# Optimization experiments

Hardware: AMD Instinct MI355X
Metric: run time of the kernel (lower is better)

The kernel has to match this reference:

```python
import jax, jax.numpy as jnp
import numpy as np

B, L, D, H, DH = 2, 2048, 768, 12, 3072
HD = D // H          # head dim = 64
EPS = 1e-6
SCALE = float(np.sqrt(HD))


def setup_inputs() -> dict:
    key = jax.random.key(0)
    ks = jax.random.split(key, 24)
    w = lambda k, shape: jax.random.normal(k, shape, jnp.float32) * 0.02
    # RoPE angles: [L, HD//2]
    inv_freq = 1.0 / (10000.0 ** (jnp.arange(HD // 2, dtype=jnp.float32) / (HD // 2)))
    ang = jnp.arange(L, dtype=jnp.float32)[:, None] * inv_freq[None, :]
    return {
        "x": jax.random.normal(ks[0], (B, L, D), jnp.float32),
        "c": jax.random.normal(ks[1], (B, D), jnp.float32),
        "freqs_cos": jnp.cos(ang),
        "freqs_sin": jnp.sin(ang),
        "W_q": w(ks[2], (D, D)), "W_k": w(ks[3], (D, D)),
        "W_v": w(ks[4], (D, D)), "W_o": w(ks[5], (D, D)),
        "cond_w1": w(ks[6], (D, DH)), "cond_b1": jnp.zeros((DH,), jnp.float32),
        "cond_w2": w(ks[7], (DH, D)), "cond_b2": jnp.zeros((D,), jnp.float32),
        "attn_norm_w": jnp.ones((D,), jnp.float32),
        "attn_alpha": w(ks[8], (D, D)), "attn_beta": w(ks[9], (D, D)),
        "attn_gamma": w(ks[10], (D, D)),
        "ffn_gate": w(ks[11], (D, DH)), "ffn_hidden": w(ks[12], (D, DH)),
        "ffn_out": w(ks[13], (DH, D)),
        "ffn_norm_w": jnp.ones((D,), jnp.float32),
        "ffn_beta": w(ks[14], (D, D)), "ffn_gamma": w(ks[15], (D, D)),
    }


def _rms_norm(x, w):
    return w * x * jax.lax.rsqrt(jnp.mean(x * x, axis=-1, keepdims=True) + EPS)


def _rope(x, cos, sin):
    # x: [b, n, l, hd]; complex pairs are consecutive (even, odd) lanes
    x0, x1 = x[..., 0::2], x[..., 1::2]
    c, s = cos[None, None], sin[None, None]          # [1,1,l,hd//2]
    r0 = x0 * c - x1 * s
    r1 = x0 * s + x1 * c
    return jnp.stack([r0, r1], axis=-1).reshape(x.shape)


def _attention(h, cos, sin, W_q, W_k, W_v, W_o):
    b, l, d = h.shape
    split = lambda y: y.reshape(b, l, H, HD).transpose(0, 2, 1, 3)  # b n l hd
    q = _rope(split(h @ W_q), cos, sin)
    k = _rope(split(h @ W_k), cos, sin)
    v = split(h @ W_v)
    scores = jnp.einsum("bnld,bnmd->bnlm", q, k) / SCALE
    attn = jax.nn.softmax(scores, axis=-1)
    o = jnp.einsum("bnlm,bnmd->bnld", attn, v)
    return o.transpose(0, 2, 1, 3).reshape(b, l, d) @ W_o


def reference(x, c, freqs_cos, freqs_sin, W_q, W_k, W_v, W_o,
              cond_w1, cond_b1, cond_w2, cond_b2,
              attn_norm_w, attn_alpha, attn_beta, attn_gamma,
              ffn_gate, ffn_hidden, ffn_out, ffn_norm_w, ffn_beta, ffn_gamma):
    # conditioning embedding
    c2 = jax.nn.silu(c @ cond_w1 + cond_b1) @ cond_w2 + cond_b2   # [b, d]
    mod = lambda W: (c2 @ W)[:, None]                              # [b, 1, d]
    # attention sub-block with AdaLN modulation + alpha gating
    h = _rms_norm(x, attn_norm_w) * mod(attn_gamma) + mod(attn_beta)
    x = x + _attention(h, freqs_cos, freqs_sin, W_q, W_k, W_v, W_o) * mod(attn_alpha)
    # SwiGLU FFN sub-block (original gates the residual by ffn_gamma, not alpha)
    h = _rms_norm(x, ffn_norm_w) * mod(ffn_gamma) + mod(ffn_beta)
    ff = (jax.nn.silu(h @ ffn_gate) * (h @ ffn_hidden)) @ ffn_out
    return x + ff * mod(ffn_gamma)
```

## Files before the change

kernel.cpp:

```cpp
#include <hip/hip_runtime.h>

typedef unsigned short u16;
typedef __attribute__((ext_vector_type(8))) short short8;
typedef __attribute__((ext_vector_type(4))) float f32x4;

#define L_SEQ 2048
#define NHEAD 12
#define KVB 128

__device__ __forceinline__ u16 f2bf(float f) {
    union { float f; unsigned u; } x; x.f = f;
    unsigned r = x.u + 0x7fffu + ((x.u >> 16) & 1u);
    return (u16)(r >> 16);
}
__device__ __forceinline__ float bf2f(u16 u) {
    union { unsigned u; float f; } x; x.u = ((unsigned)u) << 16;
    return x.f;
}
__device__ __forceinline__ float silu_f(float x) { return x / (1.f + __expf(-x)); }

__device__ __forceinline__ void gload16(const u16* g, u16* l) {
    __builtin_amdgcn_global_load_lds(
        (const __attribute__((address_space(1))) void*)g,
        (__attribute__((address_space(3))) void*)l, 16, 0, 0);
}

__global__ __launch_bounds__(256) void transpose_convert4(
    const float* __restrict__ S0, const float* __restrict__ S1,
    const float* __restrict__ S2, const float* __restrict__ S3,
    u16* __restrict__ D0, u16* __restrict__ D1, u16* __restrict__ D2, u16* __restrict__ D3,
    int K, int N)
{
    const float* W = (blockIdx.z == 0) ? S0 : (blockIdx.z == 1) ? S1 : (blockIdx.z == 2) ? S2 : S3;
    u16* Wt = (blockIdx.z == 0) ? D0 : (blockIdx.z == 1) ? D1 : (blockIdx.z == 2) ? D2 : D3;
    __shared__ float t[32][33];
    int tx = threadIdx.x & 31, ty = threadIdx.x >> 5;
    int n0 = blockIdx.x * 32, k0 = blockIdx.y * 32;
#pragma unroll
    for (int i = 0; i < 4; i++)
        t[ty + 8 * i][tx] = W[(size_t)(k0 + ty + 8 * i) * N + n0 + tx];
    __syncthreads();
#pragma unroll
    for (int i = 0; i < 4; i++)
        Wt[(size_t)(n0 + ty + 8 * i) * K + k0 + tx] = f2bf(t[tx][ty + 8 * i]);
}

__global__ __launch_bounds__(256) void cond_mlp1(
    const float* __restrict__ c, const float* __restrict__ w1, float* __restrict__ part)
{
    int j = blockIdx.x * 256 + threadIdx.x;
    int d0 = blockIdx.y * 96;
    float a0 = 0.f, a1 = 0.f;
    for (int d = d0; d < d0 + 96; ++d) {
        float w = w1[(size_t)d * 3072 + j];
        a0 += c[d] * w;
        a1 += c[768 + d] * w;
    }
    part[(size_t)(blockIdx.y * 2 + 0) * 3072 + j] = a0;
    part[(size_t)(blockIdx.y * 2 + 1) * 3072 + j] = a1;
}

__global__ __launch_bounds__(256) void cond_mlp2(
    const float* __restrict__ part, const float* __restrict__ b1,
    const float* __restrict__ w2, float* __restrict__ c2part)
{
    __shared__ float hid[2][384];
    const int tid = threadIdx.x;
    const int d0 = blockIdx.y * 384;
    for (int i = tid; i < 768; i += 256) {
        int b = i / 384, dd = i - b * 384;
        float s = b1[d0 + dd];
#pragma unroll
        for (int p = 0; p < 8; p++) s += part[(size_t)(p * 2 + b) * 3072 + d0 + dd];
        hid[b][dd] = silu_f(s);
    }
    __syncthreads();
    int jj = tid & 63, kc = tid >> 6;
    int j = blockIdx.x * 64 + jj;
    float a0 = 0.f, a1 = 0.f;
    for (int dd = kc * 96; dd < kc * 96 + 96; ++dd) {
        float w = w2[(size_t)(d0 + dd) * 768 + j];
        a0 += hid[0][dd] * w;
        a1 += hid[1][dd] * w;
    }
    __shared__ float r0[256], r1[256];
    r0[tid] = a0; r1[tid] = a1;
    __syncthreads();
    if (kc == 0) {
        a0 = r0[jj] + r0[64 + jj] + r0[128 + jj] + r0[192 + jj];
        a1 = r1[jj] + r1[64 + jj] + r1[128 + jj] + r1[192 + jj];
        c2part[(size_t)(blockIdx.y * 2 + 0) * 768 + j] = a0;
        c2part[(size_t)(blockIdx.y * 2 + 1) * 768 + j] = a1;
    }
}

__global__ __launch_bounds__(256) void mod_gemm(
    const float* __restrict__ c2part, const float* __restrict__ b2,
    const float* __restrict__ W0, const float* __restrict__ W1,
    const float* __restrict__ W2, const float* __restrict__ W3,
    const float* __restrict__ W4, float* __restrict__ out)
{
    __shared__ float c2s[2][768];
    const int tid = threadIdx.x;
    for (int i = tid; i < 1536; i += 256) {
        int b = i / 768, d = i - b * 768;
        float s = b2[d];
#pragma unroll
        for (int p = 0; p < 8; p++) s += c2part[(size_t)(p * 2 + b) * 768 + d];
        c2s[b][d] = s;
    }
    __syncthreads();
    int w = blockIdx.y;
    const float* W = (w == 0) ? W0 : (w == 1) ? W1 : (w == 2) ? W2 : (w == 3) ? W3 : W4;
    int jj = tid & 63, kc = tid >> 6;
    int j = blockIdx.x * 64 + jj;
    float a0 = 0.f, a1 = 0.f;
    for (int d = kc * 192; d < kc * 192 + 192; ++d) {
        float ww = W[(size_t)d * 768 + j];
        a0 += c2s[0][d] * ww;
        a1 += c2s[1][d] * ww;
    }
    __shared__ float r0[256], r1[256];
    r0[tid] = a0; r1[tid] = a1;
    __syncthreads();
    if (kc == 0) {
        a0 = r0[jj] + r0[64 + jj] + r0[128 + jj] + r0[192 + jj];
        a1 = r1[jj] + r1[64 + jj] + r1[128 + jj] + r1[192 + jj];
        out[(size_t)(w * 2 + 0) * 768 + j] = a0;
        out[(size_t)(w * 2 + 1) * 768 + j] = a1;
    }
}

__global__ __launch_bounds__(256) void rmsnorm_mod(
    const float* __restrict__ xin, const float* __restrict__ nw,
    const float* __restrict__ gamma, const float* __restrict__ beta,
    u16* __restrict__ hout)
{
    int row = blockIdx.x;
    int b = row >> 11;
    const float* xr = xin + (size_t)row * 768;
    int t = threadIdx.x;
    float v0 = xr[t], v1 = xr[t + 256], v2 = xr[t + 512];
    float ss = v0 * v0 + v1 * v1 + v2 * v2;
#pragma unroll
    for (int m = 1; m < 64; m <<= 1) ss += __shfl_xor(ss, m);
    __shared__ float red[4];
    if ((t & 63) == 0) red[t >> 6] = ss;
    __syncthreads();
    float tot = red[0] + red[1] + red[2] + red[3];
    float rr = rsqrtf(tot * (1.f / 768.f) + 1e-6f);
    u16* ho = hout + (size_t)row * 768;
    const float* g = gamma + (size_t)b * 768;
    const float* be = beta + (size_t)b * 768;
#pragma unroll
    for (int i = 0; i < 3; i++) {
        int col = t + i * 256;
        float v = (i == 0) ? v0 : (i == 1) ? v1 : v2;
        ho[col] = f2bf(v * rr * nw[col] * g[col] + be[col]);
    }
}

template<int BM, int WM, int MODE>
__global__ __launch_bounds__(256) void gemm_bf16(
    const u16* __restrict__ A, const u16* __restrict__ Bt,
    float* __restrict__ Cf, u16* __restrict__ Cb,
    const float* __restrict__ X, const float* __restrict__ coef,
    int M, int N, int K)
{
    constexpr int MR = WM / 16, NR = 4;
    __shared__ __align__(16) u16 As[2][BM * 32];
    __shared__ __align__(16) u16 Bs[2][128 * 32];
    const int tid = threadIdx.x;
    const int lane = tid & 63, wid = tid >> 6;
    const int lo = lane & 15, hi = lane >> 4;
    const int bm = blockIdx.x * BM, bn = blockIdx.y * 128;
    const int wrow = (wid >> 1) * WM, wcol = (wid & 1) * 64;

    f32x4 acc[MR][NR];
#pragma unroll
    for (int a = 0; a < MR; a++)
#pragma unroll
        for (int b = 0; b < NR; b++)
            acc[a][b] = (f32x4){0.f, 0.f, 0.f, 0.f};

    auto stage = [&](int buf, int k0) {
#pragma unroll
        for (int p = 0; p < BM / 64; p++) {
            int ch = tid + p * 256;
            gload16(A + (size_t)(bm + (ch >> 2)) * K + k0 + (ch & 3) * 8, &As[buf][ch * 8]);
        }
#pragma unroll
        for (int p = 0; p < 2; p++) {
            int ch = tid + p * 256;
            gload16(Bt + (size_t)(bn + (ch >> 2)) * K + k0 + (ch & 3) * 8, &Bs[buf][ch * 8]);
        }
    };

    stage(0, 0);
    int cur = 0;
    const int NT = K >> 5;
    for (int t = 0; t < NT; t++) {
        __syncthreads();
        if (t + 1 < NT) stage(cur ^ 1, (t + 1) * 32);
        short8 af[MR], bfr[NR];
#pragma unroll
        for (int mi = 0; mi < MR; mi++)
            af[mi] = *(const short8*)(&As[cur][(wrow + mi * 16 + lo) * 32 + hi * 8]);
#pragma unroll
        for (int nj = 0; nj < NR; nj++)
            bfr[nj] = *(const short8*)(&Bs[cur][(wcol + nj * 16 + lo) * 32 + hi * 8]);
        __builtin_amdgcn_s_setprio(1);
#pragma unroll
        for (int mi = 0; mi < MR; mi++)
#pragma unroll
            for (int nj = 0; nj < NR; nj++)
                acc[mi][nj] = __builtin_amdgcn_mfma_f32_16x16x32_bf16(af[mi], bfr[nj], acc[mi][nj], 0, 0, 0);
        __builtin_amdgcn_s_setprio(0);
        cur ^= 1;
    }
#pragma unroll
    for (int mi = 0; mi < MR; mi++)
#pragma unroll
        for (int nj = 0; nj < NR; nj++)
#pragma unroll
            for (int i = 0; i < 4; i++) {
                int row = bm + wrow + mi * 16 + hi * 4 + i;
                int col = bn + wcol + nj * 16 + lo;
                size_t idx = (size_t)row * N + col;
                float v = acc[mi][nj][i];
                if (MODE == 1) {
                    Cb[idx] = f2bf(v);
                } else {
                    int b = row >> 11;
                    Cf[idx] = X[idx] + v * coef[(size_t)b * N + col];
                }
            }
}

__global__ __launch_bounds__(256) void gemm_ffn1(
    const u16* __restrict__ A, const u16* __restrict__ Gt, const u16* __restrict__ Ht,
    u16* __restrict__ ff, int M, int N, int K)
{
    __shared__ __align__(16) u16 As[2][128 * 32];
    __shared__ __align__(16) u16 Gs[2][64 * 32];
    __shared__ __align__(16) u16 Hs[2][64 * 32];
    const int tid = threadIdx.x;
    const int lane = tid & 63, wid = tid >> 6;
    const int lo = lane & 15, hi = lane >> 4;
    const int bm = blockIdx.x * 128, bn = blockIdx.y * 64;
    const int wrow = (wid >> 1) * 64, wcol = (wid & 1) * 32;

    f32x4 ag[4][2], ah[4][2];
#pragma unroll
    for (int a = 0; a < 4; a++)
#pragma unroll
        for (int b = 0; b < 2; b++) {
            ag[a][b] = (f32x4){0.f, 0.f, 0.f, 0.f};
            ah[a][b] = (f32x4){0.f, 0.f, 0.f, 0.f};
        }

    auto stage = [&](int buf, int k0) {
#pragma unroll
        for (int p = 0; p < 2; p++) {
            int ch = tid + p * 256;
            gload16(A + (size_t)(bm + (ch >> 2)) * K + k0 + (ch & 3) * 8, &As[buf][ch * 8]);
        }
        {
            int ch = tid;
            gload16(Gt + (size_t)(bn + (ch >> 2)) * K + k0 + (ch & 3) * 8, &Gs[buf][ch * 8]);
            gload16(Ht + (size_t)(bn + (ch >> 2)) * K + k0 + (ch & 3) * 8, &Hs[buf][ch * 8]);
        }
    };

    stage(0, 0);
    int cur = 0;
    const int NT = K >> 5;
    for (int t = 0; t < NT; t++) {
        __syncthreads();
        if (t + 1 < NT) stage(cur ^ 1, (t + 1) * 32);
        short8 af[4], gf[2], hf[2];
#pragma unroll
        for (int mi = 0; mi < 4; mi++)
            af[mi] = *(const short8*)(&As[cur][(wrow + mi * 16 + lo) * 32 + hi * 8]);
#pragma unroll
        for (int nj = 0; nj < 2; nj++) {
            gf[nj] = *(const short8*)(&Gs[cur][(wcol + nj * 16 + lo) * 32 + hi * 8]);
            hf[nj] = *(const short8*)(&Hs[cur][(wcol + nj * 16 + lo) * 32 + hi * 8]);
        }
        __builtin_amdgcn_s_setprio(1);
#pragma unroll
        for (int mi = 0; mi < 4; mi++)
#pragma unroll
            for (int nj = 0; nj < 2; nj++) {
                ag[mi][nj] = __builtin_amdgcn_mfma_f32_16x16x32_bf16(af[mi], gf[nj], ag[mi][nj], 0, 0, 0);
                ah[mi][nj] = __builtin_amdgcn_mfma_f32_16x16x32_bf16(af[mi], hf[nj], ah[mi][nj], 0, 0, 0);
            }
        __builtin_amdgcn_s_setprio(0);
        cur ^= 1;
    }
#pragma unroll
    for (int mi = 0; mi < 4; mi++)
#pragma unroll
        for (int nj = 0; nj < 2; nj++)
#pragma unroll
            for (int i = 0; i < 4; i++) {
                int row = bm + wrow + mi * 16 + hi * 4 + i;
                int col = bn + wcol + nj * 16 + lo;
                ff[(size_t)row * N + col] = f2bf(silu_f(ag[mi][nj][i]) * ah[mi][nj][i]);
            }
}

__global__ __launch_bounds__(256) void rope_reshape(
    const u16* __restrict__ qr, const u16* __restrict__ kr, const u16* __restrict__ vr,
    const float* __restrict__ fc, const float* __restrict__ fs,
    u16* __restrict__ qo, u16* __restrict__ ko, u16* __restrict__ vt)
{
    const float QSCALE = 0.125f * 1.44269504f;
    __shared__ u16 Vl[64 * 64];
    const int tid = threadIdx.x;
    const int bh = blockIdx.y, lt = blockIdx.x;
    const int b = bh / NHEAD, h = bh % NHEAD;
    const int l0 = lt * 64;
    const int lrow = tid >> 2, ch = tid & 3;

    const size_t srow = ((size_t)(b * L_SEQ + l0 + lrow)) * 2304 + h * 64 + ch * 16;
    const size_t drow = ((size_t)(bh * L_SEQ + l0 + lrow)) * 64 + ch * 16;

    float cs[8], sn[8];
#pragma unroll
    for (int i = 0; i < 8; i++) {
        cs[i] = fc[(l0 + lrow) * 32 + ch * 8 + i];
        sn[i] = fs[(l0 + lrow) * 32 + ch * 8 + i];
    }
    union { int4 v4[2]; u16 s[16]; } iv, ov;
    iv.v4[0] = *(const int4*)(qr + srow); iv.v4[1] = *(const int4*)(qr + srow + 8);
#pragma unroll
    for (int i = 0; i < 8; i++) {
        float x0 = bf2f(iv.s[2 * i]), x1 = bf2f(iv.s[2 * i + 1]);
        ov.s[2 * i]     = f2bf((x0 * cs[i] - x1 * sn[i]) * QSCALE);
        ov.s[2 * i + 1] = f2bf((x0 * sn[i] + x1 * cs[i]) * QSCALE);
    }
    *(int4*)(qo + drow) = ov.v4[0]; *(int4*)(qo + drow + 8) = ov.v4[1];
    iv.v4[0] = *(const int4*)(kr + srow); iv.v4[1] = *(const int4*)(kr + srow + 8);
#pragma unroll
    for (int i = 0; i < 8; i++) {
        float x0 = bf2f(iv.s[2 * i]), x1 = bf2f(iv.s[2 * i + 1]);
        ov.s[2 * i]     = f2bf(x0 * cs[i] - x1 * sn[i]);
        ov.s[2 * i + 1] = f2bf(x0 * sn[i] + x1 * cs[i]);
    }
    *(int4*)(ko + drow) = ov.v4[0]; *(int4*)(ko + drow + 8) = ov.v4[1];
    iv.v4[0] = *(const int4*)(vr + srow); iv.v4[1] = *(const int4*)(vr + srow + 8);
#pragma unroll
    for (int e = 0; e < 16; e++) {
        int d = ch * 16 + e;
        Vl[d * 64 + (lrow ^ (((d >> 3) & 7) << 3))] = iv.s[e];
    }
    __syncthreads();
    const int d = tid >> 2;
    const int key = ((d >> 3) & 7) << 3;
    int4 o0 = *(const int4*)(&Vl[d * 64 + ((ch * 16) ^ key)]);
    int4 o1 = *(const int4*)(&Vl[d * 64 + ((ch * 16 + 8) ^ key)]);
    u16* vd = vt + ((size_t)bh * 64 + d) * L_SEQ + l0 + ch * 16;
    *(int4*)(vd) = o0; *(int4*)(vd + 8) = o1;
}

__global__ __launch_bounds__(256) void attn_fwd(
    const u16* __restrict__ q, const u16* __restrict__ k, const u16* __restrict__ vt,
    u16* __restrict__ outp)
{
    __shared__ __align__(16) u16 Kb[KVB * 64];
    __shared__ __align__(16) u16 Vb[64 * KVB];
    const int tid = threadIdx.x;
    const int lane = tid & 63, wid = tid >> 6;
    const int lo = lane & 15, hi = lane >> 4;
    const int lid = blockIdx.x;
    const int xcd = lid & 7, li = lid >> 3;
    const int bh = xcd * 3 + (li >> 5);
    const int qt = li & 31;
    const int b = bh / NHEAD, h = bh % NHEAD;
    const int q0 = qt * 64 + wid * 16;
    const u16* qb = q + ((size_t)bh * L_SEQ + q0) * 64;
    const u16* kbase = k + (size_t)bh * L_SEQ * 64;
    const u16* vbase = vt + (size_t)bh * 64 * L_SEQ;

    short8 qa0 = *(const short8*)(qb + lo * 64 + hi * 8);
    short8 qa1 = *(const short8*)(qb + lo * 64 + 32 + hi * 8);

    f32x4 oacc[4];
#pragma unroll
    for (int dt = 0; dt < 4; dt++) oacc[dt] = (f32x4){0.f, 0.f, 0.f, 0.f};
    float m_ = -1e30f, ls = 0.f;

    const int rk = tid >> 3, gk = tid & 7;
    const u16* ka = kbase + (size_t)rk * 64 + ((gk ^ (rk & 7)) * 8);
    const int rv = tid >> 4, gv = tid & 15;
    const u16* va = vbase + (size_t)rv * L_SEQ + ((gv ^ (rv & 15)) * 8);
    u16* kdst = &Kb[tid * 8];
    u16* vdst = &Vb[tid * 8];

    int4 kr0, kr1, kr2, kr3, vr0, vr1, vr2, vr3;
    kr0 = *(const int4*)(ka);
    kr1 = *(const int4*)(ka + 2048);
    kr2 = *(const int4*)(ka + 4096);
    kr3 = *(const int4*)(ka + 6144);
    vr0 = *(const int4*)(va);
    vr1 = *(const int4*)(va + 32768);
    vr2 = *(const int4*)(va + 65536);
    vr3 = *(const int4*)(va + 98304);

    const int NT = L_SEQ / KVB;
    u16* pw = &Kb[wid * 2048];
    const int pkey = lo << 3;
    for (int t = 0; t < NT; t++) {
        __syncthreads();
        *(int4*)(kdst)         = kr0;
        *(int4*)(kdst + 2048)  = kr1;
        *(int4*)(kdst + 4096)  = kr2;
        *(int4*)(kdst + 6144)  = kr3;
        *(int4*)(vdst)         = vr0;
        *(int4*)(vdst + 2048)  = vr1;
        *(int4*)(vdst + 4096)  = vr2;
        *(int4*)(vdst + 6144)  = vr3;
        __syncthreads();
        if (t + 1 < NT) {
            int kv0 = (t + 1) * KVB;
            const u16* kan = ka + (size_t)kv0 * 64;
            const u16* van = va + kv0;
            kr0 = *(const int4*)(kan);
            kr1 = *(const int4*)(kan + 2048);
            kr2 = *(const int4*)(kan + 4096);
            kr3 = *(const int4*)(kan + 6144);
            vr0 = *(const int4*)(van);
            vr1 = *(const int4*)(van + 32768);
            vr2 = *(const int4*)(van + 65536);
            vr3 = *(const int4*)(van + 98304);
        }
        f32x4 s[8];
#pragma unroll
        for (int nt = 0; nt < 8; nt++) {
            int kr_ = nt * 16 + lo;
            const u16* kp = &Kb[kr_ * 64];
            int key = (kr_ & 7) << 3;
            short8 kf0 = *(const short8*)(kp + ((hi * 8) ^ key));
            short8 kf1 = *(const short8*)(kp + ((32 + hi * 8) ^ key));
            __builtin_amdgcn_s_setprio(1);
            f32x4 z = (f32x4){0.f, 0.f, 0.f, 0.f};
            z = __builtin_amdgcn_mfma_f32_16x16x32_bf16(kf0, qa0, z, 0, 0, 0);
            s[nt] = __builtin_amdgcn_mfma_f32_16x16x32_bf16(kf1, qa1, s[nt] = z, 0, 0, 0);
            __builtin_amdgcn_s_setprio(0);
        }
        float t0 = fmaxf(fmaxf(s[0][0], s[0][1]), fmaxf(s[0][2], s[0][3]));
        float t1 = fmaxf(fmaxf(s[1][0], s[1][1]), fmaxf(s[1][2], s[1][3]));
        float t2 = fmaxf(fmaxf(s[2][0], s[2][1]), fmaxf(s[2][2], s[2][3]));
        float t3 = fmaxf(fmaxf(s[3][0], s[3][1]), fmaxf(s[3][2], s[3][3]));
        float t4 = fmaxf(fmaxf(s[4][0], s[4][1]), fmaxf(s[4][2], s[4][3]));
        float t5 = fmaxf(fmaxf(s[5][0], s[5][1]), fmaxf(s[5][2], s[5][3]));
        float t6 = fmaxf(fmaxf(s[6][0], s[6][1]), fmaxf(s[6][2], s[6][3]));
        float t7 = fmaxf(fmaxf(s[7][0], s[7][1]), fmaxf(s[7][2], s[7][3]));
        float pmax = fmaxf(fmaxf(fmaxf(t0, t1), fmaxf(t2, t3)),
                           fmaxf(fmaxf(t4, t5), fmaxf(t6, t7)));
        pmax = fmaxf(pmax, __shfl_xor(pmax, 16));
        pmax = fmaxf(pmax, __shfl_xor(pmax, 32));
        if (!__all(pmax - m_ <= 8.f)) {
            float mn = fmaxf(m_, pmax);
            float al = exp2f(m_ - mn);
            m_ = mn;
            ls *= al;
#pragma unroll
            for (int dt = 0; dt < 4; dt++) oacc[dt] *= al;
        }
        float rsA = 0.f, rsB = 0.f, rsC = 0.f, rsD = 0.f;
#pragma unroll
        for (int nt = 0; nt < 8; nt++) {
            float p0 = exp2f(s[nt][0] - m_);
            float p1 = exp2f(s[nt][1] - m_);
            float p2 = exp2f(s[nt][2] - m_);
            float p3 = exp2f(s[nt][3] - m_);
            s[nt][0] = p0; s[nt][1] = p1; s[nt][2] = p2; s[nt][3] = p3;
            rsA += p0; rsB += p1; rsC += p2; rsD += p3;
        }
        float rs = (rsA + rsB) + (rsC + rsD);
        rs += __shfl_xor(rs, 16);
        rs += __shfl_xor(rs, 32);
        ls += rs;
        __syncthreads();
#pragma unroll
        for (int nt = 0; nt < 8; nt++) {
            unsigned w0, w1;
            asm("v_cvt_pk_bf16_f32 %0, %1, %2" : "=v"(w0) : "v"(s[nt][0]), "v"(s[nt][1]));
            asm("v_cvt_pk_bf16_f32 %0, %1, %2" : "=v"(w1) : "v"(s[nt][2]), "v"(s[nt][3]));
            uint2 pk2; pk2.x = w0; pk2.y = w1;
            *(uint2*)(pw + lo * KVB + ((nt * 16 + hi * 4) ^ pkey)) = pk2;
        }
        short8 pa0 = *(const short8*)(pw + lo * KVB + ((0 * 32 + hi * 8) ^ pkey));
        short8 pa1 = *(const short8*)(pw + lo * KVB + ((1 * 32 + hi * 8) ^ pkey));
        short8 pa2 = *(const short8*)(pw + lo * KVB + ((2 * 32 + hi * 8) ^ pkey));
        short8 pa3 = *(const short8*)(pw + lo * KVB + ((3 * 32 + hi * 8) ^ pkey));
#pragma unroll
        for (int dt = 0; dt < 4; dt++) {
            int vr_ = dt * 16 + lo;
            const u16* vp = &Vb[vr_ * KVB];
            int vkey = (vr_ & 15) << 3;
            short8 vf0 = *(const short8*)(vp + ((0 * 32 + hi * 8) ^ vkey));
            short8 vf1 = *(const short8*)(vp + ((1 * 32 + hi * 8) ^ vkey));
            short8 vf2 = *(const short8*)(vp + ((2 * 32 + hi * 8) ^ vkey));
            short8 vf3 = *(const short8*)(vp + ((3 * 32 + hi * 8) ^ vkey));
            __builtin_amdgcn_s_setprio(1);
            oacc[dt] = __builtin_amdgcn_mfma_f32_16x16x32_bf16(vf0, pa0, oacc[dt], 0, 0, 0);
            oacc[dt] = __builtin_amdgcn_mfma_f32_16x16x32_bf16(vf1, pa1, oacc[dt], 0, 0, 0);
            oacc[dt] = __builtin_amdgcn_mfma_f32_16x16x32_bf16(vf2, pa2, oacc[dt], 0, 0, 0);
            oacc[dt] = __builtin_amdgcn_mfma_f32_16x16x32_bf16(vf3, pa3, oacc[dt], 0, 0, 0);
            __builtin_amdgcn_s_setprio(0);
        }
    }
    float inv = 1.f / ls;
    int qrow = q0 + lo;
    u16* orow = outp + ((size_t)(b * L_SEQ + qrow)) * 768 + h * 64;
#pragma unroll
    for (int dt = 0; dt < 4; dt++) {
        unsigned w0, w1;
        float o0 = oacc[dt][0] * inv, o1 = oacc[dt][1] * inv;
        float o2 = oacc[dt][2] * inv, o3 = oacc[dt][3] * inv;
        asm("v_cvt_pk_bf16_f32 %0, %1, %2" : "=v"(w0) : "v"(o0), "v"(o1));
        asm("v_cvt_pk_bf16_f32 %0, %1, %2" : "=v"(w1) : "v"(o2), "v"(o3));
        uint2 pk2; pk2.x = w0; pk2.y = w1;
        *(uint2*)(orow + dt * 16 + hi * 4) = pk2;
    }
}

extern "C" void kernel_launch(void* const* d_in, const int* in_sizes, int n_in,
                              void* d_out, int out_size, void* d_ws, size_t ws_size,
                              hipStream_t stream)
{
    const float* x      = (const float*)d_in[0];
    const float* c      = (const float*)d_in[1];
    const float* fcos   = (const float*)d_in[2];
    const float* fsin   = (const float*)d_in[3];
    const float* Wq     = (const float*)d_in[4];
    const float* Wk     = (const float*)d_in[5];
    const float* Wv     = (const float*)d_in[6];
    const float* Wo     = (const float*)d_in[7];
    const float* cw1    = (const float*)d_in[8];
    const float* cb1    = (const float*)d_in[9];
    const float* cw2    = (const float*)d_in[10];
    const float* cb2    = (const float*)d_in[11];
    const float* anw    = (const float*)d_in[12];
    const float* Walpha = (const float*)d_in[13];
    const float* Wbeta  = (const float*)d_in[14];
    const float* Wgamma = (const float*)d_in[15];
    const float* Wgate  = (const float*)d_in[16];
    const float* Whid   = (const float*)d_in[17];
    const float* Wout   = (const float*)d_in[18];
    const float* fnw    = (const float*)d_in[19];
    const float* Wbetaf = (const float*)d_in[20];
    const float* Wgammaf= (const float*)d_in[21];

    const int M = 4096;
    char* ws = (char*)d_ws;
    size_t off = 0;
    auto alloc = [&](size_t bytes) -> char* {
        char* p = ws + off;
        off += (bytes + 255) & ~(size_t)255;
        return p;
    };
    u16* wq_t   = (u16*)alloc((size_t)768 * 768 * 2);
    u16* wk_t   = (u16*)alloc((size_t)768 * 768 * 2);
    u16* wv_t   = (u16*)alloc((size_t)768 * 768 * 2);
    u16* wo_t   = (u16*)alloc((size_t)768 * 768 * 2);
    u16* gate_t = (u16*)alloc((size_t)3072 * 768 * 2);
    u16* hid_t  = (u16*)alloc((size_t)3072 * 768 * 2);
    u16* out_t  = (u16*)alloc((size_t)768 * 3072 * 2);
    float* part1 = (float*)alloc((size_t)8 * 2 * 3072 * 4);
    float* part2 = (float*)alloc((size_t)8 * 2 * 768 * 4);
    float* mods = (float*)alloc(5 * 2 * 768 * 4);
    u16* hbuf   = (u16*)alloc((size_t)M * 768 * 2);
    u16* qkvraw = (u16*)alloc((size_t)M * 2304 * 2);
    u16* qrope  = (u16*)alloc((size_t)M * 768 * 2);
    u16* krope  = (u16*)alloc((size_t)M * 768 * 2);
    u16* vtb    = (u16*)alloc((size_t)M * 768 * 2);
    u16* attnh  = (u16*)alloc((size_t)M * 768 * 2);
    float* ybuf = (float*)alloc((size_t)M * 768 * 4);
    u16* ffbuf  = (u16*)alloc((size_t)M * 3072 * 2);

    transpose_convert4<<<dim3(24, 24, 4), 256, 0, stream>>>(
        Wq, Wk, Wv, Wo, wq_t, wk_t, wv_t, wo_t, 768, 768);
    transpose_convert4<<<dim3(96, 24, 2), 256, 0, stream>>>(
        Wgate, Whid, Wgate, Whid, gate_t, hid_t, gate_t, hid_t, 768, 3072);
    transpose_convert4<<<dim3(24, 96, 1), 256, 0, stream>>>(
        Wout, Wout, Wout, Wout, out_t, out_t, out_t, out_t, 3072, 768);

    cond_mlp1<<<dim3(12, 8), 256, 0, stream>>>(c, cw1, part1);
    cond_mlp2<<<dim3(12, 8), 256, 0, stream>>>(part1, cb1, cw2, part2);
    mod_gemm<<<dim3(12, 5), 256, 0, stream>>>(
        part2, cb2, Wgamma, Wbeta, Walpha, Wgammaf, Wbetaf, mods);

    rmsnorm_mod<<<M, 256, 0, stream>>>(x, anw, mods + 0 * 1536, mods + 1 * 1536, hbuf);

    gemm_bf16<128, 64, 1><<<dim3(32, 18, 1), 256, 0, stream>>>(
        hbuf, wq_t, nullptr, qkvraw, nullptr, nullptr, M, 2304, 768);

    rope_reshape<<<dim3(32, 24), 256, 0, stream>>>(
        qkvraw, qkvraw + 768, qkvraw + 1536,
        fcos, fsin, qrope, krope, vtb);

    attn_fwd<<<dim3(768), 256, 0, stream>>>(qrope, krope, vtb, attnh);

    gemm_bf16<64, 32, 2><<<dim3(64, 6, 1), 256, 0, stream>>>(
        attnh, wo_t, ybuf, nullptr, x, mods + 2 * 1536, M, 768, 768);

    rmsnorm_mod<<<M, 256, 0, stream>>>(ybuf, fnw, mods + 3 * 1536, mods + 4 * 1536, hbuf);

    gemm_ffn1<<<dim3(32, 48), 256, 0, stream>>>(
        hbuf, gate_t, hid_t, ffbuf, M, 3072, 768);

    gemm_bf16<64, 32, 2><<<dim3(64, 6, 1), 256, 0, stream>>>(
        ffbuf, out_t, (float*)d_out, nullptr, ybuf, mods + 3 * 1536, M, 768, 3072);
}
```

Baseline: 265.4 us.

## Use 128-query attention blocks with 8 waves and a dedicated P buffer, merge transpose launches

The attention kernel now runs 512 threads per block covering 128 query rows, so each K/V tile staged in LDS is shared by twice as many queries. The tile load is split across more threads, which halves the number of registers each thread spends on prefetch. P now goes to a separate per-wave LDS buffer instead of reusing the K buffer, which lets the kernel drop one barrier per iteration. The cross-lane row-sum reduction moves out of the loop to run once at the end. The three weight transpose launches become one flat-indexed launch. In exchange, LDS use per block is higher and there are fewer blocks, which may lower occupancy.

```diff
diff --git a/kernel.cpp b/kernel.cpp
--- a/kernel.cpp
+++ b/kernel.cpp
@@ -7,6 +7,7 @@
 #define L_SEQ 2048
 #define NHEAD 12
 #define KVB 128
+#define QBLK 128
 
 __device__ __forceinline__ u16 f2bf(float f) {
     union { float f; unsigned u; } x; x.f = f;
@@ -25,17 +26,31 @@
         (__attribute__((address_space(3))) void*)l, 16, 0, 0);
 }
 
-__global__ __launch_bounds__(256) void transpose_convert4(
+__global__ __launch_bounds__(256) void transpose_all(
     const float* __restrict__ S0, const float* __restrict__ S1,
     const float* __restrict__ S2, const float* __restrict__ S3,
-    u16* __restrict__ D0, u16* __restrict__ D1, u16* __restrict__ D2, u16* __restrict__ D3,
-    int K, int N)
-{
-    const float* W = (blockIdx.z == 0) ? S0 : (blockIdx.z == 1) ? S1 : (blockIdx.z == 2) ? S2 : S3;
-    u16* Wt = (blockIdx.z == 0) ? D0 : (blockIdx.z == 1) ? D1 : (blockIdx.z == 2) ? D2 : D3;
+    const float* __restrict__ S4, const float* __restrict__ S5,
+    const float* __restrict__ S6,
+    u16* __restrict__ D0, u16* __restrict__ D1, u16* __restrict__ D2,
+    u16* __restrict__ D3, u16* __restrict__ D4, u16* __restrict__ D5,
+    u16* __restrict__ D6)
+{
+    int id = blockIdx.x;
+    const float* W; u16* Wt; int K, N, local;
+    if (id < 2304) {
+        int sec = id / 576; local = id - sec * 576; K = 768; N = 768;
+        W  = (sec == 0) ? S0 : (sec == 1) ? S1 : (sec == 2) ? S2 : S3;
+        Wt = (sec == 0) ? D0 : (sec == 1) ? D1 : (sec == 2) ? D2 : D3;
+    } else if (id < 6912) {
+        int sec = (id - 2304) / 2304; local = (id - 2304) - sec * 2304; K = 768; N = 3072;
+        W = sec ? S5 : S4; Wt = sec ? D5 : D4;
+    } else {
+        local = id - 6912; K = 3072; N = 768; W = S6; Wt = D6;
+    }
+    int nx = N >> 5;
+    int n0 = (local % nx) * 32, k0 = (local / nx) * 32;
     __shared__ float t[32][33];
     int tx = threadIdx.x & 31, ty = threadIdx.x >> 5;
-    int n0 = blockIdx.x * 32, k0 = blockIdx.y * 32;
 #pragma unroll
     for (int i = 0; i < 4; i++)
         t[ty + 8 * i][tx] = W[(size_t)(k0 + ty + 8 * i) * N + n0 + tx];
@@ -364,21 +379,22 @@
     *(int4*)(vd) = o0; *(int4*)(vd + 8) = o1;
 }
 
-__global__ __launch_bounds__(256) void attn_fwd(
+__global__ __launch_bounds__(512) void attn_fwd(
     const u16* __restrict__ q, const u16* __restrict__ k, const u16* __restrict__ vt,
     u16* __restrict__ outp)
 {
     __shared__ __align__(16) u16 Kb[KVB * 64];
     __shared__ __align__(16) u16 Vb[64 * KVB];
+    __shared__ __align__(16) u16 Ps[8][16 * KVB];
     const int tid = threadIdx.x;
     const int lane = tid & 63, wid = tid >> 6;
     const int lo = lane & 15, hi = lane >> 4;
     const int lid = blockIdx.x;
     const int xcd = lid & 7, li = lid >> 3;
-    const int bh = xcd * 3 + (li >> 5);
-    const int qt = li & 31;
+    const int bh = xcd * 3 + (li >> 4);
+    const int qt = li & 15;
     const int b = bh / NHEAD, h = bh % NHEAD;
-    const int q0 = qt * 64 + wid * 16;
+    const int q0 = qt * QBLK + wid * 16;
     const u16* qb = q + ((size_t)bh * L_SEQ + q0) * 64;
     const u16* kbase = k + (size_t)bh * L_SEQ * 64;
     const u16* vbase = vt + (size_t)bh * 64 * L_SEQ;
@@ -398,42 +414,30 @@
     u16* kdst = &Kb[tid * 8];
     u16* vdst = &Vb[tid * 8];
 
-    int4 kr0, kr1, kr2, kr3, vr0, vr1, vr2, vr3;
+    int4 kr0, kr1, vr0, vr1;
     kr0 = *(const int4*)(ka);
-    kr1 = *(const int4*)(ka + 2048);
-    kr2 = *(const int4*)(ka + 4096);
-    kr3 = *(const int4*)(ka + 6144);
+    kr1 = *(const int4*)(ka + 4096);
     vr0 = *(const int4*)(va);
-    vr1 = *(const int4*)(va + 32768);
-    vr2 = *(const int4*)(va + 65536);
-    vr3 = *(const int4*)(va + 98304);
+    vr1 = *(const int4*)(va + 65536);
 
     const int NT = L_SEQ / KVB;
-    u16* pw = &Kb[wid * 2048];
+    u16* pw = &Ps[wid][0];
     const int pkey = lo << 3;
     for (int t = 0; t < NT; t++) {
         __syncthreads();
-        *(int4*)(kdst)         = kr0;
-        *(int4*)(kdst + 2048)  = kr1;
-        *(int4*)(kdst + 4096)  = kr2;
-        *(int4*)(kdst + 6144)  = kr3;
-        *(int4*)(vdst)         = vr0;
-        *(int4*)(vdst + 2048)  = vr1;
-        *(int4*)(vdst + 4096)  = vr2;
-        *(int4*)(vdst + 6144)  = vr3;
+        *(int4*)(kdst)        = kr0;
+        *(int4*)(kdst + 4096) = kr1;
+        *(int4*)(vdst)        = vr0;
+        *(int4*)(vdst + 4096) = vr1;
         __syncthreads();
         if (t + 1 < NT) {
             int kv0 = (t + 1) * KVB;
             const u16* kan = ka + (size_t)kv0 * 64;
             const u16* van = va + kv0;
             kr0 = *(const int4*)(kan);
-            kr1 = *(const int4*)(kan + 2048);
-            kr2 = *(const int4*)(kan + 4096);
-            kr3 = *(const int4*)(kan + 6144);
+            kr1 = *(const int4*)(kan + 4096);
             vr0 = *(const int4*)(van);
-            vr1 = *(const int4*)(van + 32768);
-            vr2 = *(const int4*)(van + 65536);
-            vr3 = *(const int4*)(van + 98304);
+            vr1 = *(const int4*)(van + 65536);
         }
         f32x4 s[8];
 #pragma unroll
@@ -479,11 +483,7 @@
             s[nt][0] = p0; s[nt][1] = p1; s[nt][2] = p2; s[nt][3] = p3;
             rsA += p0; rsB += p1; rsC += p2; rsD += p3;
         }
-        float rs = (rsA + rsB) + (rsC + rsD);
-        rs += __shfl_xor(rs, 16);
-        rs += __shfl_xor(rs, 32);
-        ls += rs;
-        __syncthreads();
+        ls += (rsA + rsB) + (rsC + rsD);
 #pragma unroll
         for (int nt = 0; nt < 8; nt++) {
             unsigned w0, w1;
@@ -513,6 +513,8 @@
             __builtin_amdgcn_s_setprio(0);
         }
     }
+    ls += __shfl_xor(ls, 16);
+    ls += __shfl_xor(ls, 32);
     float inv = 1.f / ls;
     int qrow = q0 + lo;
     u16* orow = outp + ((size_t)(b * L_SEQ + qrow)) * 768 + h * 64;
@@ -582,12 +584,9 @@
     float* ybuf = (float*)alloc((size_t)M * 768 * 4);
     u16* ffbuf  = (u16*)alloc((size_t)M * 3072 * 2);
 
-    transpose_convert4<<<dim3(24, 24, 4), 256, 0, stream>>>(
-        Wq, Wk, Wv, Wo, wq_t, wk_t, wv_t, wo_t, 768, 768);
-    transpose_convert4<<<dim3(96, 24, 2), 256, 0, stream>>>(
-        Wgate, Whid, Wgate, Whid, gate_t, hid_t, gate_t, hid_t, 768, 3072);
-    transpose_convert4<<<dim3(24, 96, 1), 256, 0, stream>>>(
-        Wout, Wout, Wout, Wout, out_t, out_t, out_t, out_t, 3072, 768);
+    transpose_all<<<9216, 256, 0, stream>>>(
+        Wq, Wk, Wv, Wo, Wgate, Whid, Wout,
+        wq_t, wk_t, wv_t, wo_t, gate_t, hid_t, out_t);
 
     cond_mlp1<<<dim3(12, 8), 256, 0, stream>>>(c, cw1, part1);
     cond_mlp2<<<dim3(12, 8), 256, 0, stream>>>(part1, cb1, cw2, part2);
@@ -603,7 +602,7 @@
         qkvraw, qkvraw + 768, qkvraw + 1536,
         fcos, fsin, qrope, krope, vtb);
 
-    attn_fwd<<<dim3(768), 256, 0, stream>>>(qrope, krope, vtb, attnh);
+    attn_fwd<<<dim3(384), 512, 0, stream>>>(qrope, krope, vtb, attnh);
 
     gemm_bf16<64, 32, 2><<<dim3(64, 6, 1), 256, 0, stream>>>(
         attnh, wo_t, ybuf, nullptr, x, mods + 2 * 1536, M, 768, 768);
```

After: 260.8 us. About the same (-1.7%).
